# Kernel tuning notes

Hardware: AMD Instinct MI355X
Metric: run time of the kernel (lower is better)

The kernel has to match this reference:

```python
import jax, jax.numpy as jnp
import numpy as np

EPS = 1e-5  # torch BatchNorm2d default eps


def _conv(x, w, b, pad):
    y = jax.lax.conv_general_dilated(
        x, w, window_strides=(1, 1), padding=[(pad, pad), (pad, pad)],
        dimension_numbers=('NCHW', 'OIHW', 'NCHW'))
    return y + b[None, :, None, None]


def _bn_train(x, gamma, beta):
    # training-mode BatchNorm2d: biased batch statistics over (N,H,W)
    m = jnp.mean(x, axis=(0, 2, 3), keepdims=True)
    v = jnp.var(x, axis=(0, 2, 3), keepdims=True)
    xn = (x - m) * jax.lax.rsqrt(v + EPS)
    return xn * gamma[None, :, None, None] + beta[None, :, None, None]


def _ncc(s, t):
    # Vectorized equivalent of the per-pixel double loop.
    # ncc[b,0,i,j] = mean(tt * ss / (tt_std * ss_std)) over (C,th,tw)
    #             = sum(tt * s_sub) / (N * tt_std * ss_std)   (since sum(tt)=0)
    b, c, sh, sw = s.shape
    th, tw = t.shape[2], t.shape[3]
    N = c * th * tw
    tt = t - jnp.mean(t, axis=(1, 2, 3), keepdims=True)
    # torch.std is unbiased (divides by N-1)
    tt_std = jnp.sqrt(jnp.sum(tt * tt, axis=(1, 2, 3), keepdims=True) / (N - 1))

    # cross[b] = valid correlation of s[b] with its own template tt[b]
    def per_sample(si, ti):
        return jax.lax.conv_general_dilated(
            si[None], ti[None], (1, 1), 'VALID',
            dimension_numbers=('NCHW', 'OIHW', 'NCHW'))[0]  # (1,h,w)

    cross = jax.vmap(per_sample)(s, tt)  # (b,1,h,w)

    # per-window mean/std of s via box-filter conv over all C channels jointly
    box = jnp.ones((1, c, th, tw), dtype=s.dtype)
    win_sum = jax.lax.conv_general_dilated(
        s, box, (1, 1), 'VALID', dimension_numbers=('NCHW', 'OIHW', 'NCHW'))
    win_sqsum = jax.lax.conv_general_dilated(
        s * s, box, (1, 1), 'VALID', dimension_numbers=('NCHW', 'OIHW', 'NCHW'))
    win_mean = win_sum / N
    ss_var = jnp.maximum(win_sqsum - N * win_mean * win_mean, 0.0) / (N - 1)
    ss_std = jnp.sqrt(ss_var)

    return cross / (N * tt_std * ss_std)  # (b,1,h,w)


def reference(s, t, w1, b1, g1, be1, w2, b2, g2, be2,
              w3, b3, g3, be3, w4, b4):
    s = _bn_train(_conv(s, w1, b1, pad=1), g1, be1)
    t = _bn_train(_conv(t, w2, b2, pad=1), g2, be2)
    ncc = _ncc(s, t)
    x = _bn_train(_conv(ncc, w3, b3, pad=0), g3, be3)
    x = jax.nn.relu(x)
    return _conv(x, w4, b4, pad=0)  # (b,2,h,w)


def setup_inputs() -> dict:
    key = jax.random.key(0)
    ks = jax.random.split(key, 12)
    C = 256
    inp = {
        's': jax.random.normal(ks[0], (16, C, 64, 64), jnp.float32),
        't': jax.random.normal(ks[1], (16, C, 16, 16), jnp.float32),
        'w1': jax.random.normal(ks[2], (C, C, 3, 3), jnp.float32) * 0.02,
        'b1': jax.random.normal(ks[3], (C,), jnp.float32) * 0.02,
        'g1': jnp.ones((C,), jnp.float32),
        'be1': jnp.zeros((C,), jnp.float32),
        'w2': jax.random.normal(ks[4], (C, C, 3, 3), jnp.float32) * 0.02,
        'b2': jax.random.normal(ks[5], (C,), jnp.float32) * 0.02,
        'g2': jnp.ones((C,), jnp.float32),
        'be2': jnp.zeros((C,), jnp.float32),
        'w3': jax.random.normal(ks[6], (1, 1, 1, 1), jnp.float32),
        'b3': jax.random.normal(ks[7], (1,), jnp.float32) * 0.02,
        'g3': jnp.ones((1,), jnp.float32),
        'be3': jnp.zeros((1,), jnp.float32),
        'w4': jax.random.normal(ks[8], (2, 1, 1, 1), jnp.float32),
        'b4': jax.random.normal(ks[9], (2,), jnp.float32) * 0.02,
    }
    return inp
```

## Files before the change

### kernel.cpp

```cpp
#include <hip/hip_runtime.h>
#include <hip/hip_bf16.h>

#define EPSV 1e-5f

constexpr int B_ = 16, C_ = 256;
constexpr int OHW_ = 49 * 49;
constexpr int NTOT = 256 * 16 * 16;
constexpr int GROUPS = 32, CPERG = 8;

typedef short bf16x8 __attribute__((ext_vector_type(8)));
typedef float f32x4 __attribute__((ext_vector_type(4)));

constexpr size_t OFF_S1 = 0;
constexpr size_t SZ_S1  = (size_t)16 * 256 * 4096;
constexpr size_t OFF_T2 = OFF_S1 + SZ_S1;
constexpr size_t SZ_T2  = (size_t)16 * 256 * 256;
constexpr size_t OFF_ST = OFF_T2 + SZ_T2;
constexpr size_t OFF_Z  = OFF_ST + 2048;
constexpr size_t OFF_C  = OFF_Z + 131072;
constexpr size_t SPC_BYTES = (size_t)16 * 66 * 66 * 256 * 2;
constexpr size_t TPC_BYTES = (size_t)16 * 18 * 18 * 256 * 2;
constexpr size_t WR_BYTES  = (size_t)9 * 256 * 256 * 2;
constexpr size_t CPOFF = 0;
constexpr size_t NCOFF = CPOFF + (size_t)GROUPS * 16 * OHW_;
constexpr size_t SATOFF = NCOFF + (size_t)16 * OHW_;

__device__ __forceinline__ void gload_lds16(const void* g, void* l) {
    __builtin_amdgcn_global_load_lds((const __attribute__((address_space(1))) unsigned int*)g,
                                     (__attribute__((address_space(3))) unsigned int*)l,
                                     16, 0, 0);
}

template<int W>
__device__ __forceinline__ void pad_body(int bid, const float* __restrict__ in,
                                         __hip_bfloat16* __restrict__ outp, float* tile)
{
    constexpr int PW = W + 2;
    int icg = bid & 3; bid >>= 2;
    int yp = bid % PW; bid /= PW;
    int b = bid;
    int ic0 = icg * 64;
    int tid = threadIdx.x;
    bool interior = (yp >= 1 && yp <= W);
    if (interior) {
        int y = yp - 1;
        for (int idx = tid; idx < 64 * W; idx += 256) {
            int i = idx / W, x = idx % W;
            tile[i * (W + 1) + x] = in[(((size_t)(b * C_ + ic0 + i)) * W + y) * W + x];
        }
    }
    __syncthreads();
    for (int idx = tid; idx < PW * 16; idx += 256) {
        int xp = idx >> 4, i4 = idx & 15;
        ushort4 v = make_ushort4(0, 0, 0, 0);
        if (interior && xp >= 1 && xp <= W) {
            #pragma unroll
            for (int k = 0; k < 4; ++k) {
                __hip_bfloat16 h = __float2bfloat16(tile[(i4 * 4 + k) * (W + 1) + xp - 1]);
                reinterpret_cast<unsigned short*>(&v)[k] = *reinterpret_cast<unsigned short*>(&h);
            }
        }
        *reinterpret_cast<ushort4*>(&outp[(((size_t)(b * PW) + yp) * PW + xp) * 256 + ic0 + i4 * 4]) = v;
    }
}

__global__ __launch_bounds__(256)
void pad_all(const float* __restrict__ s, const float* __restrict__ t,
             __hip_bfloat16* __restrict__ SPc, __hip_bfloat16* __restrict__ TPc)
{
    __shared__ float tile[64 * 65];
    if (blockIdx.x < 16 * 66 * 4) pad_body<64>(blockIdx.x, s, SPc, tile);
    else                          pad_body<16>(blockIdx.x - 16 * 66 * 4, t, TPc, tile);
}

__global__ __launch_bounds__(256)
void weight_reorg_all(const float* __restrict__ w1, const float* __restrict__ w2,
                      __hip_bfloat16* __restrict__ wr1, __hip_bfloat16* __restrict__ wr2)
{
    int bb = blockIdx.x;
    const float* w = (bb < 256) ? w1 : w2;
    __hip_bfloat16* wr = (bb < 256) ? wr1 : wr2;
    int idx = (bb & 255) * 256 + threadIdx.x;
    const float* src = w + (size_t)idx * 9;
    #pragma unroll
    for (int t = 0; t < 9; ++t)
        wr[(size_t)t * 65536 + idx] = __float2bfloat16(src[t]);
}

template<int W>
__device__ __forceinline__ void conv_body(
    int logical,
    const __hip_bfloat16* __restrict__ SPc, const __hip_bfloat16* __restrict__ Wr,
    const float* __restrict__ bias, float* __restrict__ out,
    float* __restrict__ csum, float* __restrict__ csq,
    __hip_bfloat16 (&A_lds)[2][4096], __hip_bfloat16 (&B_lds)[2][4096])
{
    constexpr int PW = W + 2;
    constexpr int NPIX = W * W;
    constexpr int NT = NPIX / 128;
    int nt = logical % NT; logical /= NT;
    int mt = logical & 1;  logical >>= 1;
    int b  = logical;
    int tid = threadIdx.x;
    int lane = tid & 63;
    int wv = tid >> 6, wm = wv >> 1, wn = wv & 1;
    int oc0 = mt * 128, p0 = nt * 128;

    f32x4 acc[4][4];
    #pragma unroll
    for (int i = 0; i < 4; ++i)
        #pragma unroll
        for (int j = 0; j < 4; ++j)
            #pragma unroll
            for (int r = 0; r < 4; ++r) acc[i][j][r] = 0.f;

    int colb = lane >> 4, rA = lane & 15;
    const __hip_bfloat16* baseA[2];
    const __hip_bfloat16* baseB[2];
    #pragma unroll
    for (int it = 0; it < 2; ++it) {
        int sIdx = tid + it * 256;
        int row = sIdx >> 2, seg = sIdx & 3;
        baseA[it] = Wr + ((size_t)(oc0 + row)) * 256 + seg * 8;
        int p = p0 + row;
        int y = p / W, x = p % W;
        baseB[it] = SPc + (((size_t)(b * PW + y)) * PW + x) * 256 + seg * 8;
    }

    auto STAGE = [&](int buf, int kc) {
        int tap = kc >> 3, icc = kc & 7;
        int offA = tap * 65536 + icc * 32;
        int offB = ((tap / 3) * PW + (tap % 3)) * 256 + icc * 32;
        #pragma unroll
        for (int it = 0; it < 2; ++it) {
            int sIdx = tid + it * 256;
            gload_lds16(baseA[it] + offA, &A_lds[buf][sIdx * 8]);
            gload_lds16(baseB[it] + offB, &B_lds[buf][sIdx * 8]);
        }
    };

    STAGE(0, 0);
    asm volatile("s_waitcnt vmcnt(0)" ::: "memory");
    __syncthreads();

    for (int kc = 0; kc < 72; ++kc) {
        int cur = kc & 1;
        if (kc + 1 < 72) STAGE(cur ^ 1, kc + 1);

        const bf16x8* Af = reinterpret_cast<const bf16x8*>(&A_lds[cur][0]);
        const bf16x8* Bf = reinterpret_cast<const bf16x8*>(&B_lds[cur][0]);
        bf16x8 a[4], bb[4];
        #pragma unroll
        for (int mi = 0; mi < 4; ++mi)
            a[mi] = Af[(wm * 64 + mi * 16 + rA) * 4 + colb];
        #pragma unroll
        for (int ni = 0; ni < 4; ++ni)
            bb[ni] = Bf[(wn * 64 + ni * 16 + rA) * 4 + colb];
        #pragma unroll
        for (int mi = 0; mi < 4; ++mi)
            #pragma unroll
            for (int ni = 0; ni < 4; ++ni)
                acc[mi][ni] = __builtin_amdgcn_mfma_f32_16x16x32_bf16(
                    a[mi], bb[ni], acc[mi][ni], 0, 0, 0);

        __syncthreads();
    }

    #pragma unroll
    for (int mi = 0; mi < 4; ++mi) {
        int ocb = oc0 + wm * 64 + mi * 16 + colb * 4;
        #pragma unroll
        for (int r = 0; r < 4; ++r) {
            int oc = ocb + r;
            float bv = bias[oc];
            float* orow = out + ((size_t)(b * C_ + oc)) * NPIX;
            float s_oc = 0.f, q_oc = 0.f;
            #pragma unroll
            for (int ni = 0; ni < 4; ++ni) {
                int px = p0 + wn * 64 + ni * 16 + rA;
                float v = acc[mi][ni][r] + bv;
                orow[px] = v;
                s_oc += v; q_oc += v * v;
            }
            #pragma unroll
            for (int m_ = 1; m_ < 16; m_ <<= 1) {
                s_oc += __shfl_xor(s_oc, m_);
                q_oc += __shfl_xor(q_oc, m_);
            }
            if (rA == 0) {
                atomicAdd(&csum[oc], s_oc);
                atomicAdd(&csq[oc], q_oc);
            }
        }
    }
}

__global__ __launch_bounds__(256, 4)
void conv_all(const __hip_bfloat16* __restrict__ SPc, const __hip_bfloat16* __restrict__ Wr1,
              const float* __restrict__ b1, float* __restrict__ S1,
              float* __restrict__ CHS1, float* __restrict__ CHQ1,
              const __hip_bfloat16* __restrict__ TPc, const __hip_bfloat16* __restrict__ Wr2,
              const float* __restrict__ b2, float* __restrict__ T2,
              float* __restrict__ CHS2, float* __restrict__ CHQ2)
{
    __shared__ __hip_bfloat16 A_lds[2][4096];
    __shared__ __hip_bfloat16 B_lds[2][4096];
    int bid = blockIdx.x;
    if (bid < 64) {
        conv_body<16>(bid, TPc, Wr2, b2, T2, CHS2, CHQ2, A_lds, B_lds);
    } else {
        int l = bid - 64;
        int logical = (l & 7) * 128 + (l >> 3);
        conv_body<64>(logical, SPc, Wr1, b1, S1, CHS1, CHQ1, A_lds, B_lds);
    }
}

__device__ inline void blk_reduce2(float& a, float& q, int tid) {
    #pragma unroll
    for (int off = 32; off > 0; off >>= 1) {
        a += __shfl_down(a, off);
        q += __shfl_down(q, off);
    }
    __shared__ float ra[4], rq[4];
    if ((tid & 63) == 0) { ra[tid >> 6] = a; rq[tid >> 6] = q; }
    __syncthreads();
    if (tid == 0) { a = ra[0] + ra[1] + ra[2] + ra[3]; q = rq[0] + rq[1] + rq[2] + rq[3]; }
}

__global__ __launch_bounds__(256)
void bn_t2_stats(float* __restrict__ T2, const float* __restrict__ csum,
                 const float* __restrict__ csq, const float* __restrict__ g2,
                 const float* __restrict__ be2, float* __restrict__ tmean,
                 float* __restrict__ ttstd)
{
    __shared__ float SC[256], SH[256];
    int b = blockIdx.x, tid = threadIdx.x;
    {
        float m = csum[tid] * (1.f / 4096.f);
        float v = csq[tid] * (1.f / 4096.f) - m * m;
        float sc = rsqrtf(v + EPSV) * g2[tid];
        SC[tid] = sc; SH[tid] = be2[tid] - m * sc;
    }
    __syncthreads();
    float4* p = reinterpret_cast<float4*>(T2 + (size_t)b * NTOT);
    float s = 0.f, q = 0.f;
    for (int i4 = tid; i4 < NTOT / 4; i4 += 256) {
        int c = i4 >> 6;
        float sc = SC[c], sh = SH[c];
        float4 v = p[i4];
        v.x = v.x * sc + sh; v.y = v.y * sc + sh;
        v.z = v.z * sc + sh; v.w = v.w * sc + sh;
        s += v.x + v.y + v.z + v.w;
        q += v.x * v.x + v.y * v.y + v.z * v.z + v.w * v.w;
        p[i4] = v;
    }
    blk_reduce2(s, q, tid);
    if (tid == 0) {
        float m = s / (float)NTOT;
        tmean[b] = m;
        ttstd[b] = sqrtf(fmaxf(q - (float)NTOT * m * m, 0.f) / (float)(NTOT - 1));
    }
}

__global__ __launch_bounds__(256, 2)
void cross_v3(const float* __restrict__ s1, const float* __restrict__ t2,
              const float* __restrict__ csum, const float* __restrict__ csq,
              const float* __restrict__ g1, const float* __restrict__ be1,
              float* __restrict__ cpart, float* __restrict__ z)
{
    __shared__ float4 spl4[1024];
    __shared__ float tpl[256];
    __shared__ float red[4][64][49];

    int g = blockIdx.x & (GROUPS - 1);
    int b = blockIdx.x / GROUPS;
    int tid = threadIdx.x;
    int phase = tid >> 6;
    int lane = tid & 63;
    int i = lane;
    int i_ld = i < 49 ? i : 48;

    float acc[49];
    #pragma unroll
    for (int j = 0; j < 49; ++j) acc[j] = 0.f;
    float4 zs[4], zq[4];
    #pragma unroll
    for (int k = 0; k < 4; ++k) {
        zs[k] = make_float4(0.f, 0.f, 0.f, 0.f);
        zq[k] = make_float4(0.f, 0.f, 0.f, 0.f);
    }

    #pragma unroll 1
    for (int cc = 0; cc < CPERG; ++cc) {
        int c = g * CPERG + cc;
        float m = csum[c] * (1.f / 65536.f);
        float v = csq[c] * (1.f / 65536.f) - m * m;
        float sc = rsqrtf(v + EPSV) * g1[c];
        float sh = be1[c] - m * sc;
        __syncthreads();
        const float4* sp4 = reinterpret_cast<const float4*>(s1 + ((size_t)(b * C_ + c)) * 4096);
        #pragma unroll
        for (int k = 0; k < 4; ++k) {
            int gidx = tid + k * 256;
            float4 val = sp4[gidx];
            val.x = val.x * sc + sh; val.y = val.y * sc + sh;
            val.z = val.z * sc + sh; val.w = val.w * sc + sh;
            zs[k].x += val.x; zs[k].y += val.y; zs[k].z += val.z; zs[k].w += val.w;
            zq[k].x += val.x * val.x; zq[k].y += val.y * val.y;
            zq[k].z += val.z * val.z; zq[k].w += val.w * val.w;
            int row = gidx >> 4, jg = gidx & 15;
            spl4[row * 16 + (jg ^ (row & 7))] = val;
        }
        tpl[tid] = t2[((size_t)(b * C_ + c)) * 256 + tid];
        __syncthreads();
        #pragma unroll 1
        for (int tyl = 0; tyl < 4; ++tyl) {
            int ty = phase * 4 + tyl;
            int row = i_ld + ty;
            float r_[64];
            #pragma unroll
            for (int jg = 0; jg < 16; ++jg) {
                float4 v4 = spl4[row * 16 + (jg ^ (row & 7))];
                r_[jg * 4 + 0] = v4.x; r_[jg * 4 + 1] = v4.y;
                r_[jg * 4 + 2] = v4.z; r_[jg * 4 + 3] = v4.w;
            }
            float tt[16];
            const float4* tp4 = reinterpret_cast<const float4*>(&tpl[ty * 16]);
            #pragma unroll
            for (int k = 0; k < 4; ++k) {
                float4 tv = tp4[k];
                tt[k * 4 + 0] = tv.x; tt[k * 4 + 1] = tv.y;
                tt[k * 4 + 2] = tv.z; tt[k * 4 + 3] = tv.w;
            }
            #pragma unroll
            for (int tx = 0; tx < 16; ++tx)
                #pragma unroll
                for (int j = 0; j < 49; ++j)
                    acc[j] += tt[tx] * r_[j + tx];
        }
    }
    #pragma unroll
    for (int k = 0; k < 4; ++k) {
        int pxb = (tid + k * 256) * 4;
        float* zb  = z + (size_t)b * 4096 + pxb;
        float* z2b = z + 65536 + (size_t)b * 4096 + pxb;
        atomicAdd(&zb[0], zs[k].x);  atomicAdd(&zb[1], zs[k].y);
        atomicAdd(&zb[2], zs[k].z);  atomicAdd(&zb[3], zs[k].w);
        atomicAdd(&z2b[0], zq[k].x); atomicAdd(&z2b[1], zq[k].y);
        atomicAdd(&z2b[2], zq[k].z); atomicAdd(&z2b[3], zq[k].w);
    }
    __syncthreads();
    if (i < 49) {
        #pragma unroll
        for (int j = 0; j < 49; ++j) red[phase][i][j] = acc[j];
    }
    __syncthreads();
    float* dst = cpart + ((size_t)(g * B_ + b)) * OHW_;
    for (int e = tid; e < OHW_; e += 256) {
        int ii = e / 49, jj = e - ii * 49;
        dst[e] = red[0][ii][jj] + red[1][ii][jj] + red[2][ii][jj] + red[3][ii][jj];
    }
}

__global__ __launch_bounds__(256)
void sat_kernel(const float* __restrict__ zin, float* __restrict__ sat)
{
    __shared__ float t[65][66];
    int pl = blockIdx.x;
    int tid = threadIdx.x;
    const float* src = zin + (size_t)pl * 4096;
    for (int idx = tid; idx < 4096; idx += 256) {
        int y = idx >> 6, x = idx & 63;
        t[y + 1][x + 1] = src[idx];
    }
    for (int idx = tid; idx < 65; idx += 256) { t[0][idx] = 0.f; t[idx][0] = 0.f; }
    __syncthreads();
    if (tid < 64) {
        float run = 0.f;
        for (int x = 1; x <= 64; ++x) { run += t[tid + 1][x]; t[tid + 1][x] = run; }
    }
    __syncthreads();
    if (tid < 64) {
        float run = 0.f;
        for (int y = 1; y <= 64; ++y) { run += t[y][tid + 1]; t[y][tid + 1] = run; }
    }
    __syncthreads();
    float* dst = sat + (size_t)pl * 4225;
    for (int idx = tid; idx < 4225; idx += 256) {
        int r = idx / 65, c = idx % 65;
        dst[idx] = t[r][c];
    }
}

__global__ __launch_bounds__(256)
void ncc_kernel(const float* __restrict__ cpart, const float* __restrict__ sat,
                const float* __restrict__ tmean, const float* __restrict__ ttstd,
                float* __restrict__ ncc, float* __restrict__ s3)
{
    int idx = blockIdx.x * 256 + threadIdx.x;
    float val = 0.f;
    if (idx < B_ * OHW_) {
        int b = idx / OHW_, r = idx - b * OHW_;
        int i = r / 49, j = r - i * 49;
        float cr = 0.f;
        #pragma unroll 4
        for (int g = 0; g < GROUPS; ++g) cr += cpart[((size_t)(g * B_ + b)) * OHW_ + r];
        const float* sz = sat + (size_t)b * 4225;
        const float* sq = sat + (size_t)(16 + b) * 4225;
        int a00 = i * 65 + j, a01 = i * 65 + j + 16;
        int a10 = (i + 16) * 65 + j, a11 = (i + 16) * 65 + j + 16;
        float wsum = sz[a11] - sz[a01] - sz[a10] + sz[a00];
        float wq   = sq[a11] - sq[a01] - sq[a10] + sq[a00];
        float crosst = cr - tmean[b] * wsum;
        float ssvar = fmaxf(wq - wsum * wsum * (1.f / 65536.f), 0.f) * (1.f / 65535.f);
        float ssstd = sqrtf(ssvar);
        val = crosst / (65536.f * ttstd[b] * ssstd);
        ncc[idx] = val;
    }
    float s = val, q = val * val;
    blk_reduce2(s, q, threadIdx.x);
    if (threadIdx.x == 0) { atomicAdd(&s3[0], s); atomicAdd(&s3[1], q); }
}

__global__ __launch_bounds__(256)
void final_kernel(const float* __restrict__ ncc, const float* __restrict__ s3,
                  const float* __restrict__ w3, const float* __restrict__ b3,
                  const float* __restrict__ g3, const float* __restrict__ be3,
                  const float* __restrict__ w4, const float* __restrict__ b4,
                  float* __restrict__ out)
{
    int idx = blockIdx.x * 256 + threadIdx.x;
    if (idx >= B_ * OHW_) return;
    constexpr float M = (float)(B_ * OHW_);
    float mn = s3[0] / M;
    float vn = s3[1] / M - mn * mn;
    float W3 = w3[0], B3 = b3[0];
    float my = W3 * mn + B3;
    float vy = W3 * W3 * vn;
    float sc = rsqrtf(vy + EPSV) * g3[0];
    float y = (W3 * ncc[idx] + B3 - my) * sc + be3[0];
    float h = fmaxf(y, 0.f);
    int b = idx / OHW_, r = idx - b * OHW_;
    out[((size_t)(b * 2 + 0)) * OHW_ + r] = h * w4[0] + b4[0];
    out[((size_t)(b * 2 + 1)) * OHW_ + r] = h * w4[1] + b4[1];
}

extern "C" void kernel_launch(void* const* d_in, const int* in_sizes, int n_in,
                              void* d_out, int out_size, void* d_ws, size_t ws_size,
                              hipStream_t stream)
{
    const float* s   = (const float*)d_in[0];
    const float* t   = (const float*)d_in[1];
    const float* w1  = (const float*)d_in[2];
    const float* b1  = (const float*)d_in[3];
    const float* g1  = (const float*)d_in[4];
    const float* be1 = (const float*)d_in[5];
    const float* w2  = (const float*)d_in[6];
    const float* b2  = (const float*)d_in[7];
    const float* g2  = (const float*)d_in[8];
    const float* be2 = (const float*)d_in[9];
    const float* w3  = (const float*)d_in[10];
    const float* b3  = (const float*)d_in[11];
    const float* g3  = (const float*)d_in[12];
    const float* be3 = (const float*)d_in[13];
    const float* w4  = (const float*)d_in[14];
    const float* b4  = (const float*)d_in[15];

    float* ws = (float*)d_ws;
    float* S1 = ws + OFF_S1;
    float* T2 = ws + OFF_T2;
    float* ST = ws + OFF_ST;
    float* CHS1 = ST + 0;
    float* CHQ1 = ST + 256;
    float* CHS2 = ST + 512;
    float* CHQ2 = ST + 768;
    float* S3   = ST + 1024;
    float* TM   = ST + 1040;
    float* TSD  = ST + 1056;
    float* Z    = ws + OFF_Z;

    char* Cb = (char*)(ws + OFF_C);
    __hip_bfloat16* SPc = (__hip_bfloat16*)Cb;
    __hip_bfloat16* TPc = (__hip_bfloat16*)(Cb + SPC_BYTES);
    __hip_bfloat16* Wr1 = (__hip_bfloat16*)(Cb + SPC_BYTES + TPC_BYTES);
    __hip_bfloat16* Wr2 = (__hip_bfloat16*)(Cb + SPC_BYTES + TPC_BYTES + WR_BYTES);
    float* Cf = (float*)Cb;
    float* CP  = Cf + CPOFF;
    float* NC  = Cf + NCOFF;
    float* SAT = Cf + SATOFF;

    hipMemsetAsync(ST, 0, (2048 + 131072) * sizeof(float), stream);

    pad_all<<<dim3(16 * 66 * 4 + 16 * 18 * 4), dim3(256), 0, stream>>>(s, t, SPc, TPc);
    weight_reorg_all<<<dim3(512), dim3(256), 0, stream>>>(w1, w2, Wr1, Wr2);

    conv_all<<<dim3(64 + 1024), dim3(256), 0, stream>>>(SPc, Wr1, b1, S1, CHS1, CHQ1,
                                                        TPc, Wr2, b2, T2, CHS2, CHQ2);

    bn_t2_stats<<<dim3(16), dim3(256), 0, stream>>>(T2, CHS2, CHQ2, g2, be2, TM, TSD);

    cross_v3<<<dim3(16 * GROUPS), dim3(256), 0, stream>>>(S1, T2, CHS1, CHQ1, g1, be1, CP, Z);
    sat_kernel<<<dim3(32), dim3(256), 0, stream>>>(Z, SAT);
    ncc_kernel<<<dim3(151), dim3(256), 0, stream>>>(CP, SAT, TM, TSD, NC, S3);
    final_kernel<<<dim3(151), dim3(256), 0, stream>>>(NC, S3, w3, b3, g3, be3, w4, b4, (float*)d_out);
}
```

Before: 453.4 us.

## Single-buffer conv LDS staging and merge weight reorg into pad kernel

The bf16 MFMA conv loop drops its double-buffered LDS staging and now loads each K-chunk into a single buffer, waiting for the loads and a barrier before computing. Source addresses are recomputed every iteration instead of coming from precomputed bases. The launch-bounds occupancy hint is removed and LDS use is halved, which may allow more resident blocks. The weight reorganisation kernel is folded into the pad kernel to save a launch. In exchange, global-load latency is no longer hidden behind the MFMA work.

```diff
diff --git a/kernel.cpp b/kernel.cpp
--- a/kernel.cpp
+++ b/kernel.cpp
@@ -66,25 +66,24 @@
 
 __global__ __launch_bounds__(256)
 void pad_all(const float* __restrict__ s, const float* __restrict__ t,
-             __hip_bfloat16* __restrict__ SPc, __hip_bfloat16* __restrict__ TPc)
+             __hip_bfloat16* __restrict__ SPc, __hip_bfloat16* __restrict__ TPc,
+             const float* __restrict__ w1, const float* __restrict__ w2,
+             __hip_bfloat16* __restrict__ wr1, __hip_bfloat16* __restrict__ wr2)
 {
     __shared__ float tile[64 * 65];
-    if (blockIdx.x < 16 * 66 * 4) pad_body<64>(blockIdx.x, s, SPc, tile);
-    else                          pad_body<16>(blockIdx.x - 16 * 66 * 4, t, TPc, tile);
-}
-
-__global__ __launch_bounds__(256)
-void weight_reorg_all(const float* __restrict__ w1, const float* __restrict__ w2,
-                      __hip_bfloat16* __restrict__ wr1, __hip_bfloat16* __restrict__ wr2)
-{
-    int bb = blockIdx.x;
-    const float* w = (bb < 256) ? w1 : w2;
-    __hip_bfloat16* wr = (bb < 256) ? wr1 : wr2;
-    int idx = (bb & 255) * 256 + threadIdx.x;
+    constexpr int NP1 = 16 * 66 * 4, NP2 = 16 * 18 * 4;
+    int bid = blockIdx.x;
+    if (bid < NP1) { pad_body<64>(bid, s, SPc, tile); return; }
+    bid -= NP1;
+    if (bid < NP2) { pad_body<16>(bid, t, TPc, tile); return; }
+    bid -= NP2;
+    const float* w = (bid < 256) ? w1 : w2;
+    __hip_bfloat16* wr = (bid < 256) ? wr1 : wr2;
+    int idx = (bid & 255) * 256 + threadIdx.x;
     const float* src = w + (size_t)idx * 9;
     #pragma unroll
-    for (int t = 0; t < 9; ++t)
-        wr[(size_t)t * 65536 + idx] = __float2bfloat16(src[t]);
+    for (int t_ = 0; t_ < 9; ++t_)
+        wr[(size_t)t_ * 65536 + idx] = __float2bfloat16(src[t_]);
 }
 
 template<int W>
@@ -93,7 +92,7 @@
     const __hip_bfloat16* __restrict__ SPc, const __hip_bfloat16* __restrict__ Wr,
     const float* __restrict__ bias, float* __restrict__ out,
     float* __restrict__ csum, float* __restrict__ csq,
-    __hip_bfloat16 (&A_lds)[2][4096], __hip_bfloat16 (&B_lds)[2][4096])
+    __hip_bfloat16* A_lds, __hip_bfloat16* B_lds)
 {
     constexpr int PW = W + 2;
     constexpr int NPIX = W * W;
@@ -114,41 +113,32 @@
             #pragma unroll
             for (int r = 0; r < 4; ++r) acc[i][j][r] = 0.f;
 
-    int colb = lane >> 4, rA = lane & 15;
-    const __hip_bfloat16* baseA[2];
-    const __hip_bfloat16* baseB[2];
-    #pragma unroll
-    for (int it = 0; it < 2; ++it) {
-        int sIdx = tid + it * 256;
-        int row = sIdx >> 2, seg = sIdx & 3;
-        baseA[it] = Wr + ((size_t)(oc0 + row)) * 256 + seg * 8;
-        int p = p0 + row;
-        int y = p / W, x = p % W;
-        baseB[it] = SPc + (((size_t)(b * PW + y)) * PW + x) * 256 + seg * 8;
-    }
-
-    auto STAGE = [&](int buf, int kc) {
+    const bf16x8* Af = reinterpret_cast<const bf16x8*>(A_lds);
+    const bf16x8* Bf = reinterpret_cast<const bf16x8*>(B_lds);
+    int colb = lane >> 4;
+    int rA = lane & 15;
+
+    for (int kc = 0; kc < 72; ++kc) {
         int tap = kc >> 3, icc = kc & 7;
-        int offA = tap * 65536 + icc * 32;
-        int offB = ((tap / 3) * PW + (tap % 3)) * 256 + icc * 32;
+        int ic0 = icc * 32;
+        int dy = tap / 3, dx = tap - dy * 3;
+        __syncthreads();
         #pragma unroll
         for (int it = 0; it < 2; ++it) {
             int sIdx = tid + it * 256;
-            gload_lds16(baseA[it] + offA, &A_lds[buf][sIdx * 8]);
-            gload_lds16(baseB[it] + offB, &B_lds[buf][sIdx * 8]);
-        }
-    };
-
-    STAGE(0, 0);
-    asm volatile("s_waitcnt vmcnt(0)" ::: "memory");
-    __syncthreads();
-
-    for (int kc = 0; kc < 72; ++kc) {
-        int cur = kc & 1;
-        if (kc + 1 < 72) STAGE(cur ^ 1, kc + 1);
-
-        const bf16x8* Af = reinterpret_cast<const bf16x8*>(&A_lds[cur][0]);
-        const bf16x8* Bf = reinterpret_cast<const bf16x8*>(&B_lds[cur][0]);
+            int row = sIdx >> 2, seg = sIdx & 3;
+            const __hip_bfloat16* srcA =
+                Wr + ((size_t)(tap * 256 + oc0 + row)) * 256 + ic0 + seg * 8;
+            gload_lds16(srcA, &A_lds[sIdx * 8]);
+            int p = p0 + row;
+            int y = p / W, x = p % W;
+            const __hip_bfloat16* srcB =
+                SPc + (((size_t)(b * PW + y + dy)) * PW + x + dx) * 256 + ic0 + seg * 8;
+            gload_lds16(srcB, &B_lds[sIdx * 8]);
+        }
+        asm volatile("s_waitcnt vmcnt(0)" ::: "memory");
+        __syncthreads();
+
         bf16x8 a[4], bb[4];
         #pragma unroll
         for (int mi = 0; mi < 4; ++mi)
@@ -162,8 +152,6 @@
             for (int ni = 0; ni < 4; ++ni)
                 acc[mi][ni] = __builtin_amdgcn_mfma_f32_16x16x32_bf16(
                     a[mi], bb[ni], acc[mi][ni], 0, 0, 0);
-
-        __syncthreads();
     }
 
     #pragma unroll
@@ -195,7 +183,7 @@
     }
 }
 
-__global__ __launch_bounds__(256, 4)
+__global__ __launch_bounds__(256)
 void conv_all(const __hip_bfloat16* __restrict__ SPc, const __hip_bfloat16* __restrict__ Wr1,
               const float* __restrict__ b1, float* __restrict__ S1,
               float* __restrict__ CHS1, float* __restrict__ CHQ1,
@@ -203,8 +191,8 @@
               const float* __restrict__ b2, float* __restrict__ T2,
               float* __restrict__ CHS2, float* __restrict__ CHQ2)
 {
-    __shared__ __hip_bfloat16 A_lds[2][4096];
-    __shared__ __hip_bfloat16 B_lds[2][4096];
+    __shared__ __hip_bfloat16 A_lds[4096];
+    __shared__ __hip_bfloat16 B_lds[4096];
     int bid = blockIdx.x;
     if (bid < 64) {
         conv_body<16>(bid, TPc, Wr2, b2, T2, CHS2, CHQ2, A_lds, B_lds);
@@ -491,8 +479,8 @@
 
     hipMemsetAsync(ST, 0, (2048 + 131072) * sizeof(float), stream);
 
-    pad_all<<<dim3(16 * 66 * 4 + 16 * 18 * 4), dim3(256), 0, stream>>>(s, t, SPc, TPc);
-    weight_reorg_all<<<dim3(512), dim3(256), 0, stream>>>(w1, w2, Wr1, Wr2);
+    pad_all<<<dim3(16 * 66 * 4 + 16 * 18 * 4 + 512), dim3(256), 0, stream>>>(
+        s, t, SPc, TPc, w1, w2, Wr1, Wr2);
 
     conv_all<<<dim3(64 + 1024), dim3(256), 0, stream>>>(SPc, Wr1, b1, S1, CHS1, CHQ1,
                                                         TPc, Wr2, b2, T2, CHS2, CHQ2);
```

After: 438.9 us, median of 2. -3.2%, faster.
